# Optimization experiments

Measured on AMD Instinct MI355X. Metric: run time of the kernel, lower is better.

## Reference

```python
import jax, jax.numpy as jnp
import numpy as np

N = 100000
E = 3200000
IN_C, H1, H2 = 512, 64, 32


def gcn_norm(edge_index, edge_weight, num_nodes):
    """PyG gcn_norm with add_self_loops=True: D^-1/2 (A+I) D^-1/2 edge weights."""
    row, col = edge_index[0], edge_index[1]
    loop = jnp.arange(num_nodes, dtype=edge_index.dtype)
    row = jnp.concatenate([row, loop])
    col = jnp.concatenate([col, loop])
    w = jnp.concatenate([edge_weight, jnp.ones((num_nodes,), edge_weight.dtype)])
    deg = jax.ops.segment_sum(w, col, num_segments=num_nodes)
    dinv = jnp.where(deg > 0, jax.lax.rsqrt(jnp.maximum(deg, 1e-12)), 0.0)
    wnorm = dinv[row] * w * dinv[col]
    return row, col, wnorm


def gcn_conv(x, W, b, row, col, wnorm, num_nodes):
    h = x @ W                                   # [N, out] linear first (out <= in)
    msg = wnorm[:, None] * h[row]               # gather + per-edge scale  [E+N, out]
    out = jax.ops.segment_sum(msg, col, num_segments=num_nodes)
    return out + b


def setup_inputs() -> dict:
    key = jax.random.key(0)
    ks = jax.random.split(key, 9)
    x = jax.random.normal(ks[0], (N, IN_C), dtype=jnp.float32)
    edge_index = jax.random.randint(ks[1], (2, E), 0, N, dtype=jnp.int64)
    edge_weight = jax.random.uniform(ks[2], (E,), dtype=jnp.float32)
    # Glorot-style init for GCN linear weights, zero bias (PyG defaults).
    def glorot(k, fan_in, fan_out):
        s = np.sqrt(6.0 / (fan_in + fan_out)).astype(np.float32)
        return jax.random.uniform(k, (fan_in, fan_out), jnp.float32, -s, s)
    return {
        "x": x,
        "edge_index": edge_index,
        "edge_weight": edge_weight,
        "W1": glorot(ks[3], IN_C, H1), "b1": jnp.zeros((H1,), jnp.float32),
        "W2": glorot(ks[4], H1, H2),  "b2": jnp.zeros((H2,), jnp.float32),
        "W3": glorot(ks[5], H2, 1),   "b3": jnp.zeros((1,), jnp.float32),
    }


def reference(x, edge_index, edge_weight, W1, b1, W2, b2, W3, b3):
    # Inference mode: dropout is identity (training=False).
    row, col, wnorm = gcn_norm(edge_index, edge_weight, N)  # cached=True: shared across layers
    h = jax.nn.relu(gcn_conv(x, W1, b1, row, col, wnorm, N))
    h = jax.nn.relu(gcn_conv(h, W2, b2, row, col, wnorm, N))
    h = gcn_conv(h, W3, b3, row, col, wnorm, N)
    return h.reshape(-1)  # [N]
```

## Files before the change

kernel.cpp:

```cpp
#include <hip/hip_runtime.h>

constexpr int BLK = 256;
constexpr int NBLKBIN = 512;
constexpr int MAXNB   = 1024;

typedef __bf16 bf16x8 __attribute__((ext_vector_type(8)));
typedef float  f32x4  __attribute__((ext_vector_type(4)));

__device__ __forceinline__ float blo(unsigned u) { return __uint_as_float(u << 16); }
__device__ __forceinline__ float bhi(unsigned u) { return __uint_as_float(u & 0xffff0000u); }

__device__ __forceinline__ int detect64(const void* ei) {
    const int* p = (const int*)ei;
    int is64 = 1;
#pragma unroll
    for (int i = 0; i < 16; ++i)
        if (p[2 * i + 1] != 0) is64 = 0;
    return is64;
}

__device__ __forceinline__ int load_idx(const void* ei, size_t pos, int is64) {
    if (is64) return (int)((const long long*)ei)[pos];
    return ((const int*)ei)[pos];
}

__global__ void k_prep(const float* __restrict__ W1, const float* __restrict__ W2,
                       __bf16* __restrict__ Wtf, __bf16* __restrict__ Wtf2,
                       int* __restrict__ bkt_cnt, int nb) {
    const int b = blockIdx.x;
    const int t = threadIdx.x;
    if (b < 16) {
        int i = b * 256 + t;
        int lane = i & 63;
        int tt   = (i >> 6) & 3;
        int k0c  = i >> 8;
        int col  = tt * 16 + (lane & 15);
        int kbase = k0c * 32 + (lane >> 4) * 8;
        bf16x8 v;
#pragma unroll
        for (int j = 0; j < 8; ++j) v[j] = (__bf16)W1[(size_t)(kbase + j) * 64 + col];
        *(bf16x8*)(Wtf + (size_t)i * 8) = v;
    } else if (b == 16) {
        int i = t;
        int lane = i & 63;
        int ct   = i >> 6;
        int tt = ct & 1, chunk = ct >> 1;
        int col  = tt * 16 + (lane & 15);
        int kbase = chunk * 32 + (lane >> 4) * 8;
        bf16x8 v;
#pragma unroll
        for (int j = 0; j < 8; ++j) v[j] = (__bf16)W2[(size_t)(kbase + j) * 32 + col];
        *(bf16x8*)(Wtf2 + (size_t)i * 8) = v;
    } else {
        for (int i = t; i < nb; i += 256) bkt_cnt[i] = 0;
    }
}

__global__ __launch_bounds__(256) void k_binhist(const void* __restrict__ ei, int e,
                                                 int* __restrict__ bucket_cnt, int nb) {
    __shared__ int hist[MAXNB];
    const int t = threadIdx.x;
    for (int b = t; b < nb; b += 256) hist[b] = 0;
    __syncthreads();
    const int is64 = detect64(ei);
    const int chunk = (e + NBLKBIN - 1) / NBLKBIN;
    const int i0 = blockIdx.x * chunk;
    const int i1 = min(e, i0 + chunk);
    for (int i = i0 + t; i < i1; i += 256) {
        int dst = load_idx(ei, (size_t)e + i, is64);
        atomicAdd(&hist[dst >> 7], 1);
    }
    __syncthreads();
    for (int b = t; b < nb; b += 256) {
        int c = hist[b];
        if (c) atomicAdd(&bucket_cnt[b], c);
    }
}

__global__ void k_scanbkt(const int* __restrict__ cnt, int* __restrict__ offs,
                          int* __restrict__ cursor, int nb, int e) {
    __shared__ int sh[256];
    const int t = threadIdx.x;
    const int base = t * 4;
    int v[4]; int s = 0;
#pragma unroll
    for (int k = 0; k < 4; ++k) {
        int i = base + k;
        v[k] = (i < nb) ? cnt[i] : 0;
        s += v[k];
    }
    sh[t] = s;
    __syncthreads();
    for (int d = 1; d < 256; d <<= 1) {
        int x = (t >= d) ? sh[t - d] : 0;
        __syncthreads();
        sh[t] += x;
        __syncthreads();
    }
    int excl = (t == 0) ? 0 : sh[t - 1];
#pragma unroll
    for (int k = 0; k < 4; ++k) {
        int i = base + k;
        if (i < nb) { offs[i] = excl; cursor[i] = excl; excl += v[k]; }
    }
    if (t == 255) offs[nb] = e;
}

__global__ __launch_bounds__(256) void k_binscatter(const void* __restrict__ ei,
                                                    const float* __restrict__ ew, int e,
                                                    int* __restrict__ bucket_cursor,
                                                    int2* __restrict__ binned, int nb) {
    __shared__ int hist[MAXNB];
    const int t = threadIdx.x;
    for (int b = t; b < nb; b += 256) hist[b] = 0;
    __syncthreads();
    const int is64 = detect64(ei);
    const int chunk = (e + NBLKBIN - 1) / NBLKBIN;
    const int i0 = blockIdx.x * chunk;
    const int i1 = min(e, i0 + chunk);
    for (int i = i0 + t; i < i1; i += 256) {
        int dst = load_idx(ei, (size_t)e + i, is64);
        atomicAdd(&hist[dst >> 7], 1);
    }
    __syncthreads();
    for (int b = t; b < nb; b += 256) {
        int c = hist[b];
        int base = 0;
        if (c) base = atomicAdd(&bucket_cursor[b], c);
        hist[b] = base;
    }
    __syncthreads();
    for (int i = i0 + t; i < i1; i += 256) {
        int dst = load_idx(ei, (size_t)e + i, is64);
        int src = load_idx(ei, (size_t)i, is64);
        float w = ew[i];
        int bin = dst >> 7;
        int pos = atomicAdd(&hist[bin], 1);
        binned[pos] = make_int2(src | ((dst & 127) << 20), __float_as_int(w));
    }
}

__global__ __launch_bounds__(256) void k_build(const int* __restrict__ bkt_offs,
                                               const int2* __restrict__ binned,
                                               float* __restrict__ dinv,
                                               int* __restrict__ offs,
                                               int2* __restrict__ csrp, int n, int e) {
    __shared__ int                icnt[128];
    __shared__ unsigned long long facc[128];
    __shared__ int                scn[128];
    __shared__ int                cur[128];
    const int t = threadIdx.x;
    const int b = blockIdx.x;
    if (t < 128) { icnt[t] = 0; facc[t] = 0ull; }
    __syncthreads();
    const int j0 = bkt_offs[b], j1 = bkt_offs[b + 1];
    const float SCALE = 1099511627776.f;
    for (int j = j0 + t; j < j1; j += 256) {
        int2 p = binned[j];
        int dl = ((unsigned)p.x) >> 20;
        atomicAdd(&icnt[dl], 1);
        atomicAdd(&facc[dl], (unsigned long long)(__int_as_float(p.y) * SCALE));
    }
    __syncthreads();
    if (t < 128) {
        int nd = b * 128 + t;
        if (nd < n) dinv[nd] = rsqrtf(fmaf((float)facc[t], 1.f / 1099511627776.f, 1.0f));
        scn[t] = icnt[t];
    }
    __syncthreads();
    for (int d = 1; d < 128; d <<= 1) {
        int x = 0;
        if (t < 128 && t >= d) x = scn[t - d];
        __syncthreads();
        if (t < 128) scn[t] += x;
        __syncthreads();
    }
    if (t < 128) {
        int excl = (t == 0) ? 0 : scn[t - 1];
        int abs0 = j0 + excl;
        cur[t] = abs0;
        int nd = b * 128 + t;
        if (nd < n) offs[nd] = abs0;
    }
    if (b == 0 && t == 0) offs[n] = e;
    __syncthreads();
    for (int j = j0 + t; j < j1; j += 256) {
        int2 p = binned[j];
        int dl  = ((unsigned)p.x) >> 20;
        int src = p.x & 0xFFFFF;
        int pos = atomicAdd(&cur[dl], 1);
        csrp[pos] = make_int2(src, p.y);
    }
}

__global__ __launch_bounds__(256) void k_gemm1_mfma(const float* __restrict__ X,
                                                    const __bf16* __restrict__ Wtf,
                                                    const float* __restrict__ dinv,
                                                    __bf16* __restrict__ H, int nrows) {
    const int wave = threadIdx.x >> 6;
    const int lane = threadIdx.x & 63;
    const int l15  = lane & 15;
    const int lq   = lane >> 4;
    const long rbase = (long)blockIdx.x * 128 + wave * 32;

    long ar0 = rbase + l15;      if (ar0 >= nrows) ar0 = nrows - 1;
    long ar1 = rbase + 16 + l15; if (ar1 >= nrows) ar1 = nrows - 1;
    const float4* x0 = (const float4*)(X + (size_t)ar0 * 512) + lq * 2;
    const float4* x1 = (const float4*)(X + (size_t)ar1 * 512) + lq * 2;

    f32x4 acc[2][4];
#pragma unroll
    for (int r = 0; r < 2; ++r)
#pragma unroll
        for (int t = 0; t < 4; ++t) acc[r][t] = f32x4{0.f, 0.f, 0.f, 0.f};

    float4 pa[2][2][2];
#pragma unroll
    for (int s = 0; s < 2; ++s) {
        pa[s][0][0] = x0[s * 8]; pa[s][0][1] = x0[s * 8 + 1];
        pa[s][1][0] = x1[s * 8]; pa[s][1][1] = x1[s * 8 + 1];
    }

#pragma unroll
    for (int k0c = 0; k0c < 16; ++k0c) {
        const int s = k0c & 1;
        float4 a00 = pa[s][0][0], a01 = pa[s][0][1];
        float4 a10 = pa[s][1][0], a11 = pa[s][1][1];
        if (k0c + 2 < 16) {
            pa[s][0][0] = x0[(k0c + 2) * 8]; pa[s][0][1] = x0[(k0c + 2) * 8 + 1];
            pa[s][1][0] = x1[(k0c + 2) * 8]; pa[s][1][1] = x1[(k0c + 2) * 8 + 1];
        }
        bf16x8 af0, af1;
        af0[0] = (__bf16)a00.x; af0[1] = (__bf16)a00.y; af0[2] = (__bf16)a00.z; af0[3] = (__bf16)a00.w;
        af0[4] = (__bf16)a01.x; af0[5] = (__bf16)a01.y; af0[6] = (__bf16)a01.z; af0[7] = (__bf16)a01.w;
        af1[0] = (__bf16)a10.x; af1[1] = (__bf16)a10.y; af1[2] = (__bf16)a10.z; af1[3] = (__bf16)a10.w;
        af1[4] = (__bf16)a11.x; af1[5] = (__bf16)a11.y; af1[6] = (__bf16)a11.z; af1[7] = (__bf16)a11.w;
#pragma unroll
        for (int t = 0; t < 4; ++t) {
            bf16x8 bf_ = *(const bf16x8*)(Wtf + ((size_t)(k0c * 4 + t) * 64 + lane) * 8);
            acc[0][t] = __builtin_amdgcn_mfma_f32_16x16x32_bf16(af0, bf_, acc[0][t], 0, 0, 0);
            acc[1][t] = __builtin_amdgcn_mfma_f32_16x16x32_bf16(af1, bf_, acc[1][t], 0, 0, 0);
        }
    }
#pragma unroll
    for (int rr = 0; rr < 2; ++rr)
#pragma unroll
    for (int r = 0; r < 4; ++r) {
        long row = rbase + rr * 16 + lq * 4 + r;
        if (row < nrows) {
            float dv = dinv[row];
#pragma unroll
            for (int t = 0; t < 4; ++t)
                H[(size_t)row * 64 + t * 16 + l15] = (__bf16)(acc[rr][t][r] * dv);
        }
    }
}

__global__ __launch_bounds__(256) void k_gemm2_mfma(const __bf16* __restrict__ A,
                                                    const __bf16* __restrict__ Wtf2,
                                                    const float* __restrict__ dinv,
                                                    __bf16* __restrict__ H, int nrows) {
    const int wave = threadIdx.x >> 6;
    const int lane = threadIdx.x & 63;
    const int l15  = lane & 15;
    const int lq   = lane >> 4;
    const long rbase = (long)blockIdx.x * 64 + wave * 16;

    long arow = rbase + l15;
    if (arow >= nrows) arow = nrows - 1;

    f32x4 acc[2] = {{0.f,0.f,0.f,0.f},{0.f,0.f,0.f,0.f}};
#pragma unroll
    for (int c = 0; c < 2; ++c) {
        bf16x8 af = *(const bf16x8*)(A + (size_t)arow * 64 + c * 32 + lq * 8);
#pragma unroll
        for (int t = 0; t < 2; ++t) {
            bf16x8 bf_ = *(const bf16x8*)(Wtf2 + ((size_t)(c * 2 + t) * 64 + lane) * 8);
            acc[t] = __builtin_amdgcn_mfma_f32_16x16x32_bf16(af, bf_, acc[t], 0, 0, 0);
        }
    }
#pragma unroll
    for (int r = 0; r < 4; ++r) {
        long row = rbase + lq * 4 + r;
        if (row < nrows) {
            float dv = dinv[row];
#pragma unroll
            for (int t = 0; t < 2; ++t)
                H[(size_t)row * 32 + t * 16 + l15] = (__bf16)(acc[t][r] * dv);
        }
    }
}

template <int K, int EPI>
__global__ __launch_bounds__(256) void k_prop_bf(const int* __restrict__ offs,
                                                 const int2* __restrict__ csrp,
                                                 const __bf16* __restrict__ hb,
                                                 const float* __restrict__ dinv,
                                                 const float* __restrict__ bias,
                                                 const float* __restrict__ W3,
                                                 void* __restrict__ outv, int n) {
    constexpr int SUB = K / 4;
    constexpr int NPW = 64 / SUB;
    constexpr int NPB = 4 * NPW;
    const int t    = threadIdx.x;
    const int lane = t & 63;
    const int wave = t >> 6;
    const int chq  = lane & (SUB - 1);
    const int sub  = lane / SUB;
    const long nd  = (long)blockIdx.x * NPB + wave * NPW + sub;
    if (nd >= n) return;

    const unsigned short* h = (const unsigned short*)hb;
    const int j0 = offs[nd], j1 = offs[nd + 1];
    float a0 = 0.f, a1 = 0.f, a2 = 0.f, a3 = 0.f;
    int j = j0;
    for (; j + 3 < j1; j += 4) {
        int2 p0 = csrp[j];
        int2 p1 = csrp[j + 1];
        int2 p2 = csrp[j + 2];
        int2 p3 = csrp[j + 3];
        uint2 u0 = *(const uint2*)(h + (size_t)p0.x * K + 4 * chq);
        uint2 u1 = *(const uint2*)(h + (size_t)p1.x * K + 4 * chq);
        uint2 u2 = *(const uint2*)(h + (size_t)p2.x * K + 4 * chq);
        uint2 u3 = *(const uint2*)(h + (size_t)p3.x * K + 4 * chq);
        float w0 = __int_as_float(p0.y), w1 = __int_as_float(p1.y);
        float w2 = __int_as_float(p2.y), w3 = __int_as_float(p3.y);
        a0 = fmaf(w0, blo(u0.x), a0); a1 = fmaf(w0, bhi(u0.x), a1);
        a2 = fmaf(w0, blo(u0.y), a2); a3 = fmaf(w0, bhi(u0.y), a3);
        a0 = fmaf(w1, blo(u1.x), a0); a1 = fmaf(w1, bhi(u1.x), a1);
        a2 = fmaf(w1, blo(u1.y), a2); a3 = fmaf(w1, bhi(u1.y), a3);
        a0 = fmaf(w2, blo(u2.x), a0); a1 = fmaf(w2, bhi(u2.x), a1);
        a2 = fmaf(w2, blo(u2.y), a2); a3 = fmaf(w2, bhi(u2.y), a3);
        a0 = fmaf(w3, blo(u3.x), a0); a1 = fmaf(w3, bhi(u3.x), a1);
        a2 = fmaf(w3, blo(u3.y), a2); a3 = fmaf(w3, bhi(u3.y), a3);
    }
    for (; j < j1; ++j) {
        int2 p0 = csrp[j];
        uint2 u0 = *(const uint2*)(h + (size_t)p0.x * K + 4 * chq);
        float w0 = __int_as_float(p0.y);
        a0 = fmaf(w0, blo(u0.x), a0); a1 = fmaf(w0, bhi(u0.x), a1);
        a2 = fmaf(w0, blo(u0.y), a2); a3 = fmaf(w0, bhi(u0.y), a3);
    }
    const float di = dinv[nd];
    uint2 us = *(const uint2*)(h + (size_t)nd * K + 4 * chq);
    float4 bv = *(const float4*)(bias + 4 * chq);
    float o0 = fmaf(di, a0 + blo(us.x), bv.x);
    float o1 = fmaf(di, a1 + bhi(us.x), bv.y);
    float o2 = fmaf(di, a2 + blo(us.y), bv.z);
    float o3 = fmaf(di, a3 + bhi(us.y), bv.w);
    o0 = fmaxf(o0, 0.f); o1 = fmaxf(o1, 0.f); o2 = fmaxf(o2, 0.f); o3 = fmaxf(o3, 0.f);
    if (EPI == 0) {
        unsigned short s0 = __builtin_bit_cast(unsigned short, (__bf16)o0);
        unsigned short s1 = __builtin_bit_cast(unsigned short, (__bf16)o1);
        unsigned short s2 = __builtin_bit_cast(unsigned short, (__bf16)o2);
        unsigned short s3 = __builtin_bit_cast(unsigned short, (__bf16)o3);
        uint2 pk;
        pk.x = (unsigned)s0 | ((unsigned)s1 << 16);
        pk.y = (unsigned)s2 | ((unsigned)s3 << 16);
        *(uint2*)((unsigned*)outv + (size_t)nd * (K / 2) + 2 * chq) = pk;
    } else {
        float4 wv = *(const float4*)(W3 + 4 * chq);
        float part = o0 * wv.x + o1 * wv.y + o2 * wv.z + o3 * wv.w;
#pragma unroll
        for (int d = SUB / 2; d >= 1; d >>= 1) part += __shfl_xor(part, d, SUB);
        if (chq == 0) ((float*)outv)[nd] = di * part;
    }
}

__global__ __launch_bounds__(256) void k_prop1(const int* __restrict__ offs,
                                               const int2* __restrict__ csrp,
                                               const float* __restrict__ h,
                                               const float* __restrict__ dinv,
                                               const float* __restrict__ bias,
                                               float* __restrict__ out, int n) {
    long nd = (long)blockIdx.x * BLK + threadIdx.x;
    if (nd >= n) return;
    const int j0 = offs[nd], j1 = offs[nd + 1];
    float acc = 0.f;
    int j = j0;
    for (; j + 3 < j1; j += 4) {
        int2 p0 = csrp[j];
        int2 p1 = csrp[j + 1];
        int2 p2 = csrp[j + 2];
        int2 p3 = csrp[j + 3];
        acc = fmaf(__int_as_float(p0.y), h[p0.x], acc);
        acc = fmaf(__int_as_float(p1.y), h[p1.x], acc);
        acc = fmaf(__int_as_float(p2.y), h[p2.x], acc);
        acc = fmaf(__int_as_float(p3.y), h[p3.x], acc);
    }
    for (; j < j1; ++j) {
        int2 p0 = csrp[j];
        acc = fmaf(__int_as_float(p0.y), h[p0.x], acc);
    }
    const float di = dinv[nd];
    out[nd] = fmaf(di, acc + h[nd], bias[0]);
}

extern "C" void kernel_launch(void* const* d_in, const int* in_sizes, int n_in,
                              void* d_out, int out_size, void* d_ws, size_t ws_size,
                              hipStream_t stream) {
    const float* x  = (const float*)d_in[0];
    const void*  ei = d_in[1];
    const float* ew = (const float*)d_in[2];
    const float* W1 = (const float*)d_in[3];
    const float* b1 = (const float*)d_in[4];
    const float* W2 = (const float*)d_in[5];
    const float* b2 = (const float*)d_in[6];
    const float* W3 = (const float*)d_in[7];
    const float* b3 = (const float*)d_in[8];
    float* out = (float*)d_out;

    const int n = in_sizes[0] / 512;
    const int e = in_sizes[2];
    const int nb = (n + 127) >> 7;

    char* ws = (char*)d_ws;
    size_t off = 0;
    auto alloc = [&](size_t bytes) {
        void* p = ws + off;
        off = (off + bytes + 255) & ~(size_t)255;
        return p;
    };
    int2*   binned   = (int2*)  alloc((size_t)e * 8);
    __bf16* hbuf1    = (__bf16*)binned;
    int*    bkt_cnt  = (int*)   alloc((size_t)(MAXNB + 1) * 4);
    int*    bkt_offs = (int*)   alloc((size_t)(MAXNB + 1) * 4);
    int*    bkt_cur  = (int*)   alloc((size_t)(MAXNB + 1) * 4);
    int*    offs     = (int*)   alloc((size_t)(n + 1) * 4);
    int2*   csrp     = (int2*)  alloc((size_t)e * 8);
    float*  dinv     = (float*) alloc((size_t)n * 4);
    __bf16* pb64     = (__bf16*)alloc((size_t)n * 64 * 2);
    __bf16* hbuf2    = (__bf16*)alloc((size_t)n * 32 * 2);
    float*  h3       = (float*) alloc((size_t)n * 4);
    __bf16* Wtf      = (__bf16*)alloc((size_t)512 * 64 * 2);
    __bf16* Wtf2     = (__bf16*)alloc((size_t)64 * 32 * 2);
    (void)ws_size; (void)n_in; (void)out_size;

    const int gb_n = (n + BLK - 1) / BLK;

    k_prep<<<18, 256, 0, stream>>>(W1, W2, Wtf, Wtf2, bkt_cnt, nb);
    k_binhist<<<NBLKBIN, 256, 0, stream>>>(ei, e, bkt_cnt, nb);
    k_scanbkt<<<1, 256, 0, stream>>>(bkt_cnt, bkt_offs, bkt_cur, nb, e);
    k_binscatter<<<NBLKBIN, 256, 0, stream>>>(ei, ew, e, bkt_cur, binned, nb);
    k_build<<<nb, 256, 0, stream>>>(bkt_offs, binned, dinv, offs, csrp, n, e);

    k_gemm1_mfma<<<(n + 127) / 128, 256, 0, stream>>>(x, Wtf, dinv, hbuf1, n);
    k_prop_bf<64, 0><<<(n + 15) / 16, 256, 0, stream>>>(offs, csrp, hbuf1, dinv, b1, nullptr, pb64, n);

    k_gemm2_mfma<<<(n + 63) / 64, 256, 0, stream>>>(pb64, Wtf2, dinv, hbuf2, n);
    k_prop_bf<32, 1><<<(n + 31) / 32, 256, 0, stream>>>(offs, csrp, hbuf2, dinv, b2, W3, h3, n);

    k_prop1<<<gb_n, BLK, 0, stream>>>(offs, csrp, h3, dinv, b3, out, n);
}
```

Baseline: 326.9 us.

## Fuse edge binning with GEMM1, compute degrees early, prefold normalization into edge weights

Degree accumulation now happens with global float atomics during the histogram pass, so dinv is ready before CSR construction. With dinv no longer needed by GEMM1, the bin-scatter and GEMM1 run as one kernel whose blocks are split between the two jobs, letting the bandwidth-heavy matmul overlap the scatter. The symmetric normalization dinv[src]*w*dinv[dst] is folded into the stored CSR weights, which removes the dinv scaling from the GEMM epilogues and the propagation kernels. In exchange it adds E global atomics on deg and a separate buffer for H1, which is no longer aliased onto the binned array, and float atomics make the degree sums order-dependent.

```diff
diff --git a/kernel.cpp b/kernel.cpp
--- a/kernel.cpp
+++ b/kernel.cpp
@@ -26,7 +26,8 @@
 
 __global__ void k_prep(const float* __restrict__ W1, const float* __restrict__ W2,
                        __bf16* __restrict__ Wtf, __bf16* __restrict__ Wtf2,
-                       int* __restrict__ bkt_cnt, int nb) {
+                       int* __restrict__ bkt_cnt, int nb,
+                       float* __restrict__ deg, int n) {
     const int b = blockIdx.x;
     const int t = threadIdx.x;
     if (b < 16) {
@@ -51,13 +52,18 @@
 #pragma unroll
         for (int j = 0; j < 8; ++j) v[j] = (__bf16)W2[(size_t)(kbase + j) * 32 + col];
         *(bf16x8*)(Wtf2 + (size_t)i * 8) = v;
+    } else if (b == 17) {
+        for (int i = t; i < nb; i += 256) bkt_cnt[i] = 0;
     } else {
-        for (int i = t; i < nb; i += 256) bkt_cnt[i] = 0;
-    }
-}
-
-__global__ __launch_bounds__(256) void k_binhist(const void* __restrict__ ei, int e,
-                                                 int* __restrict__ bucket_cnt, int nb) {
+        int i = (b - 18) * 256 + t;
+        if (i < n) deg[i] = 0.f;
+    }
+}
+
+__global__ __launch_bounds__(256) void k_binhist_deg(const void* __restrict__ ei,
+                                                     const float* __restrict__ ew, int e,
+                                                     int* __restrict__ bucket_cnt, int nb,
+                                                     float* __restrict__ deg) {
     __shared__ int hist[MAXNB];
     const int t = threadIdx.x;
     for (int b = t; b < nb; b += 256) hist[b] = 0;
@@ -69,6 +75,7 @@
     for (int i = i0 + t; i < i1; i += 256) {
         int dst = load_idx(ei, (size_t)e + i, is64);
         atomicAdd(&hist[dst >> 7], 1);
+        atomicAdd(&deg[dst], ew[i]);
     }
     __syncthreads();
     for (int b = t; b < nb; b += 256) {
@@ -77,131 +84,85 @@
     }
 }
 
-__global__ void k_scanbkt(const int* __restrict__ cnt, int* __restrict__ offs,
-                          int* __restrict__ cursor, int nb, int e) {
+__global__ void k_scan_rsqrt(const int* __restrict__ cnt, int* __restrict__ offs,
+                             int* __restrict__ cursor, int nb, int e,
+                             const float* __restrict__ deg, float* __restrict__ dinv, int n) {
     __shared__ int sh[256];
     const int t = threadIdx.x;
-    const int base = t * 4;
-    int v[4]; int s = 0;
-#pragma unroll
-    for (int k = 0; k < 4; ++k) {
-        int i = base + k;
-        v[k] = (i < nb) ? cnt[i] : 0;
-        s += v[k];
-    }
-    sh[t] = s;
-    __syncthreads();
-    for (int d = 1; d < 256; d <<= 1) {
-        int x = (t >= d) ? sh[t - d] : 0;
-        __syncthreads();
-        sh[t] += x;
-        __syncthreads();
-    }
-    int excl = (t == 0) ? 0 : sh[t - 1];
-#pragma unroll
-    for (int k = 0; k < 4; ++k) {
-        int i = base + k;
-        if (i < nb) { offs[i] = excl; cursor[i] = excl; excl += v[k]; }
-    }
-    if (t == 255) offs[nb] = e;
-}
-
-__global__ __launch_bounds__(256) void k_binscatter(const void* __restrict__ ei,
-                                                    const float* __restrict__ ew, int e,
-                                                    int* __restrict__ bucket_cursor,
-                                                    int2* __restrict__ binned, int nb) {
+    if (blockIdx.x == 0) {
+        const int base = t * 4;
+        int v[4]; int s = 0;
+#pragma unroll
+        for (int k = 0; k < 4; ++k) {
+            int i = base + k;
+            v[k] = (i < nb) ? cnt[i] : 0;
+            s += v[k];
+        }
+        sh[t] = s;
+        __syncthreads();
+        for (int d = 1; d < 256; d <<= 1) {
+            int x = (t >= d) ? sh[t - d] : 0;
+            __syncthreads();
+            sh[t] += x;
+            __syncthreads();
+        }
+        int excl = (t == 0) ? 0 : sh[t - 1];
+#pragma unroll
+        for (int k = 0; k < 4; ++k) {
+            int i = base + k;
+            if (i < nb) { offs[i] = excl; cursor[i] = excl; excl += v[k]; }
+        }
+        if (t == 255) offs[nb] = e;
+    } else {
+        long i = (long)(blockIdx.x - 1) * BLK + t;
+        if (i < n) dinv[i] = rsqrtf(1.0f + deg[i]);
+    }
+}
+
+__global__ __launch_bounds__(256) void k_fat(const void* __restrict__ ei,
+                                             const float* __restrict__ ew, int e,
+                                             int* __restrict__ bucket_cursor,
+                                             int2* __restrict__ binned, int nb,
+                                             const float* __restrict__ X,
+                                             const __bf16* __restrict__ Wtf,
+                                             __bf16* __restrict__ H, int nrows) {
     __shared__ int hist[MAXNB];
     const int t = threadIdx.x;
-    for (int b = t; b < nb; b += 256) hist[b] = 0;
-    __syncthreads();
-    const int is64 = detect64(ei);
-    const int chunk = (e + NBLKBIN - 1) / NBLKBIN;
-    const int i0 = blockIdx.x * chunk;
-    const int i1 = min(e, i0 + chunk);
-    for (int i = i0 + t; i < i1; i += 256) {
-        int dst = load_idx(ei, (size_t)e + i, is64);
-        atomicAdd(&hist[dst >> 7], 1);
-    }
-    __syncthreads();
-    for (int b = t; b < nb; b += 256) {
-        int c = hist[b];
-        int base = 0;
-        if (c) base = atomicAdd(&bucket_cursor[b], c);
-        hist[b] = base;
-    }
-    __syncthreads();
-    for (int i = i0 + t; i < i1; i += 256) {
-        int dst = load_idx(ei, (size_t)e + i, is64);
-        int src = load_idx(ei, (size_t)i, is64);
-        float w = ew[i];
-        int bin = dst >> 7;
-        int pos = atomicAdd(&hist[bin], 1);
-        binned[pos] = make_int2(src | ((dst & 127) << 20), __float_as_int(w));
-    }
-}
-
-__global__ __launch_bounds__(256) void k_build(const int* __restrict__ bkt_offs,
-                                               const int2* __restrict__ binned,
-                                               float* __restrict__ dinv,
-                                               int* __restrict__ offs,
-                                               int2* __restrict__ csrp, int n, int e) {
-    __shared__ int                icnt[128];
-    __shared__ unsigned long long facc[128];
-    __shared__ int                scn[128];
-    __shared__ int                cur[128];
-    const int t = threadIdx.x;
-    const int b = blockIdx.x;
-    if (t < 128) { icnt[t] = 0; facc[t] = 0ull; }
-    __syncthreads();
-    const int j0 = bkt_offs[b], j1 = bkt_offs[b + 1];
-    const float SCALE = 1099511627776.f;
-    for (int j = j0 + t; j < j1; j += 256) {
-        int2 p = binned[j];
-        int dl = ((unsigned)p.x) >> 20;
-        atomicAdd(&icnt[dl], 1);
-        atomicAdd(&facc[dl], (unsigned long long)(__int_as_float(p.y) * SCALE));
-    }
-    __syncthreads();
-    if (t < 128) {
-        int nd = b * 128 + t;
-        if (nd < n) dinv[nd] = rsqrtf(fmaf((float)facc[t], 1.f / 1099511627776.f, 1.0f));
-        scn[t] = icnt[t];
-    }
-    __syncthreads();
-    for (int d = 1; d < 128; d <<= 1) {
-        int x = 0;
-        if (t < 128 && t >= d) x = scn[t - d];
-        __syncthreads();
-        if (t < 128) scn[t] += x;
-        __syncthreads();
-    }
-    if (t < 128) {
-        int excl = (t == 0) ? 0 : scn[t - 1];
-        int abs0 = j0 + excl;
-        cur[t] = abs0;
-        int nd = b * 128 + t;
-        if (nd < n) offs[nd] = abs0;
-    }
-    if (b == 0 && t == 0) offs[n] = e;
-    __syncthreads();
-    for (int j = j0 + t; j < j1; j += 256) {
-        int2 p = binned[j];
-        int dl  = ((unsigned)p.x) >> 20;
-        int src = p.x & 0xFFFFF;
-        int pos = atomicAdd(&cur[dl], 1);
-        csrp[pos] = make_int2(src, p.y);
-    }
-}
-
-__global__ __launch_bounds__(256) void k_gemm1_mfma(const float* __restrict__ X,
-                                                    const __bf16* __restrict__ Wtf,
-                                                    const float* __restrict__ dinv,
-                                                    __bf16* __restrict__ H, int nrows) {
-    const int wave = threadIdx.x >> 6;
-    const int lane = threadIdx.x & 63;
+    if (blockIdx.x < NBLKBIN) {
+        for (int b = t; b < nb; b += 256) hist[b] = 0;
+        __syncthreads();
+        const int is64 = detect64(ei);
+        const int chunk = (e + NBLKBIN - 1) / NBLKBIN;
+        const int i0 = blockIdx.x * chunk;
+        const int i1 = min(e, i0 + chunk);
+        for (int i = i0 + t; i < i1; i += 256) {
+            int dst = load_idx(ei, (size_t)e + i, is64);
+            atomicAdd(&hist[dst >> 7], 1);
+        }
+        __syncthreads();
+        for (int b = t; b < nb; b += 256) {
+            int c = hist[b];
+            int base = 0;
+            if (c) base = atomicAdd(&bucket_cursor[b], c);
+            hist[b] = base;
+        }
+        __syncthreads();
+        for (int i = i0 + t; i < i1; i += 256) {
+            int dst = load_idx(ei, (size_t)e + i, is64);
+            int src = load_idx(ei, (size_t)i, is64);
+            float w = ew[i];
+            int bin = dst >> 7;
+            int pos = atomicAdd(&hist[bin], 1);
+            binned[pos] = make_int2(src | ((dst & 127) << 20), __float_as_int(w));
+        }
+        return;
+    }
+    const int bid  = blockIdx.x - NBLKBIN;
+    const int wave = t >> 6;
+    const int lane = t & 63;
     const int l15  = lane & 15;
     const int lq   = lane >> 4;
-    const long rbase = (long)blockIdx.x * 128 + wave * 32;
+    const long rbase = (long)bid * 128 + wave * 32;
 
     long ar0 = rbase + l15;      if (ar0 >= nrows) ar0 = nrows - 1;
     long ar1 = rbase + 16 + l15; if (ar1 >= nrows) ar1 = nrows - 1;
@@ -212,7 +173,7 @@
 #pragma unroll
     for (int r = 0; r < 2; ++r)
 #pragma unroll
-        for (int t = 0; t < 4; ++t) acc[r][t] = f32x4{0.f, 0.f, 0.f, 0.f};
+        for (int tt = 0; tt < 4; ++tt) acc[r][tt] = f32x4{0.f, 0.f, 0.f, 0.f};
 
     float4 pa[2][2][2];
 #pragma unroll
@@ -236,29 +197,76 @@
         af1[0] = (__bf16)a10.x; af1[1] = (__bf16)a10.y; af1[2] = (__bf16)a10.z; af1[3] = (__bf16)a10.w;
         af1[4] = (__bf16)a11.x; af1[5] = (__bf16)a11.y; af1[6] = (__bf16)a11.z; af1[7] = (__bf16)a11.w;
 #pragma unroll
-        for (int t = 0; t < 4; ++t) {
-            bf16x8 bf_ = *(const bf16x8*)(Wtf + ((size_t)(k0c * 4 + t) * 64 + lane) * 8);
-            acc[0][t] = __builtin_amdgcn_mfma_f32_16x16x32_bf16(af0, bf_, acc[0][t], 0, 0, 0);
-            acc[1][t] = __builtin_amdgcn_mfma_f32_16x16x32_bf16(af1, bf_, acc[1][t], 0, 0, 0);
+        for (int tt = 0; tt < 4; ++tt) {
+            bf16x8 bf_ = *(const bf16x8*)(Wtf + ((size_t)(k0c * 4 + tt) * 64 + lane) * 8);
+            acc[0][tt] = __builtin_amdgcn_mfma_f32_16x16x32_bf16(af0, bf_, acc[0][tt], 0, 0, 0);
+            acc[1][tt] = __builtin_amdgcn_mfma_f32_16x16x32_bf16(af1, bf_, acc[1][tt], 0, 0, 0);
         }
     }
 #pragma unroll
     for (int rr = 0; rr < 2; ++rr)
+#pragma unroll
+    for (int tt = 0; tt < 4; ++tt)
 #pragma unroll
     for (int r = 0; r < 4; ++r) {
         long row = rbase + rr * 16 + lq * 4 + r;
-        if (row < nrows) {
-            float dv = dinv[row];
-#pragma unroll
-            for (int t = 0; t < 4; ++t)
-                H[(size_t)row * 64 + t * 16 + l15] = (__bf16)(acc[rr][t][r] * dv);
-        }
+        if (row < nrows) H[(size_t)row * 64 + tt * 16 + l15] = (__bf16)acc[rr][tt][r];
+    }
+}
+
+__global__ __launch_bounds__(256) void k_build(const int* __restrict__ bkt_offs,
+                                               const int2* __restrict__ binned,
+                                               const float* __restrict__ dinv,
+                                               int* __restrict__ offs,
+                                               int2* __restrict__ csrp, int n, int e) {
+    __shared__ int   icnt[128];
+    __shared__ int   scn[128];
+    __shared__ int   cur[128];
+    __shared__ float ddst[128];
+    const int t = threadIdx.x;
+    const int b = blockIdx.x;
+    if (t < 128) {
+        icnt[t] = 0;
+        int nd = b * 128 + t;
+        ddst[t] = (nd < n) ? dinv[nd] : 0.f;
+    }
+    __syncthreads();
+    const int j0 = bkt_offs[b], j1 = bkt_offs[b + 1];
+    for (int j = j0 + t; j < j1; j += 256) {
+        int2 p = binned[j];
+        atomicAdd(&icnt[((unsigned)p.x) >> 20], 1);
+    }
+    __syncthreads();
+    if (t < 128) scn[t] = icnt[t];
+    __syncthreads();
+    for (int d = 1; d < 128; d <<= 1) {
+        int x = 0;
+        if (t < 128 && t >= d) x = scn[t - d];
+        __syncthreads();
+        if (t < 128) scn[t] += x;
+        __syncthreads();
+    }
+    if (t < 128) {
+        int excl = (t == 0) ? 0 : scn[t - 1];
+        int abs0 = j0 + excl;
+        cur[t] = abs0;
+        int nd = b * 128 + t;
+        if (nd < n) offs[nd] = abs0;
+    }
+    if (b == 0 && t == 0) offs[n] = e;
+    __syncthreads();
+    for (int j = j0 + t; j < j1; j += 256) {
+        int2 p = binned[j];
+        int dl  = ((unsigned)p.x) >> 20;
+        int src = p.x & 0xFFFFF;
+        int pos = atomicAdd(&cur[dl], 1);
+        float w2 = __int_as_float(p.y) * dinv[src] * ddst[dl];
+        csrp[pos] = make_int2(src, __float_as_int(w2));
     }
 }
 
 __global__ __launch_bounds__(256) void k_gemm2_mfma(const __bf16* __restrict__ A,
                                                     const __bf16* __restrict__ Wtf2,
-                                                    const float* __restrict__ dinv,
                                                     __bf16* __restrict__ H, int nrows) {
     const int wave = threadIdx.x >> 6;
     const int lane = threadIdx.x & 63;
@@ -280,14 +288,11 @@
         }
     }
 #pragma unroll
+    for (int t = 0; t < 2; ++t)
+#pragma unroll
     for (int r = 0; r < 4; ++r) {
         long row = rbase + lq * 4 + r;
-        if (row < nrows) {
-            float dv = dinv[row];
-#pragma unroll
-            for (int t = 0; t < 2; ++t)
-                H[(size_t)row * 32 + t * 16 + l15] = (__bf16)(acc[t][r] * dv);
-        }
+        if (row < nrows) H[(size_t)row * 32 + t * 16 + l15] = (__bf16)acc[t][r];
     }
 }
 
@@ -342,12 +347,13 @@
         a2 = fmaf(w0, blo(u0.y), a2); a3 = fmaf(w0, bhi(u0.y), a3);
     }
     const float di = dinv[nd];
+    const float s  = di * di;
     uint2 us = *(const uint2*)(h + (size_t)nd * K + 4 * chq);
     float4 bv = *(const float4*)(bias + 4 * chq);
-    float o0 = fmaf(di, a0 + blo(us.x), bv.x);
-    float o1 = fmaf(di, a1 + bhi(us.x), bv.y);
-    float o2 = fmaf(di, a2 + blo(us.y), bv.z);
-    float o3 = fmaf(di, a3 + bhi(us.y), bv.w);
+    float o0 = fmaf(s, blo(us.x), a0 + bv.x);
+    float o1 = fmaf(s, bhi(us.x), a1 + bv.y);
+    float o2 = fmaf(s, blo(us.y), a2 + bv.z);
+    float o3 = fmaf(s, bhi(us.y), a3 + bv.w);
     o0 = fmaxf(o0, 0.f); o1 = fmaxf(o1, 0.f); o2 = fmaxf(o2, 0.f); o3 = fmaxf(o3, 0.f);
     if (EPI == 0) {
         unsigned short s0 = __builtin_bit_cast(unsigned short, (__bf16)o0);
@@ -363,7 +369,7 @@
         float part = o0 * wv.x + o1 * wv.y + o2 * wv.z + o3 * wv.w;
 #pragma unroll
         for (int d = SUB / 2; d >= 1; d >>= 1) part += __shfl_xor(part, d, SUB);
-        if (chq == 0) ((float*)outv)[nd] = di * part;
+        if (chq == 0) ((float*)outv)[nd] = part;
     }
 }
 
@@ -393,7 +399,7 @@
         acc = fmaf(__int_as_float(p0.y), h[p0.x], acc);
     }
     const float di = dinv[nd];
-    out[nd] = fmaf(di, acc + h[nd], bias[0]);
+    out[nd] = fmaf(di * di, h[nd], acc + bias[0]);
 }
 
 extern "C" void kernel_launch(void* const* d_in, const int* in_sizes, int n_in,
@@ -428,27 +434,27 @@
     int*    bkt_cur  = (int*)   alloc((size_t)(MAXNB + 1) * 4);
     int*    offs     = (int*)   alloc((size_t)(n + 1) * 4);
     int2*   csrp     = (int2*)  alloc((size_t)e * 8);
+    float*  deg      = (float*) alloc((size_t)n * 4);
     float*  dinv     = (float*) alloc((size_t)n * 4);
+    __bf16* hb1      = (__bf16*)alloc((size_t)n * 64 * 2);
     __bf16* pb64     = (__bf16*)alloc((size_t)n * 64 * 2);
     __bf16* hbuf2    = (__bf16*)alloc((size_t)n * 32 * 2);
     float*  h3       = (float*) alloc((size_t)n * 4);
     __bf16* Wtf      = (__bf16*)alloc((size_t)512 * 64 * 2);
     __bf16* Wtf2     = (__bf16*)alloc((size_t)64 * 32 * 2);
-    (void)ws_size; (void)n_in; (void)out_size;
+    (void)ws_size; (void)n_in; (void)out_size; (void)hbuf1;
 
     const int gb_n = (n + BLK - 1) / BLK;
 
-    k_prep<<<18, 256, 0, stream>>>(W1, W2, Wtf, Wtf2, bkt_cnt, nb);
-    k_binhist<<<NBLKBIN, 256, 0, stream>>>(ei, e, bkt_cnt, nb);
-    k_scanbkt<<<1, 256, 0, stream>>>(bkt_cnt, bkt_offs, bkt_cur, nb, e);
-    k_binscatter<<<NBLKBIN, 256, 0, stream>>>(ei, ew, e, bkt_cur, binned, nb);
+    k_prep<<<18 + gb_n, 256, 0, stream>>>(W1, W2, Wtf, Wtf2, bkt_cnt, nb, deg, n);
+    k_binhist_deg<<<NBLKBIN, 256, 0, stream>>>(ei, ew, e, bkt_cnt, nb, deg);
+    k_scan_rsqrt<<<1 + gb_n, 256, 0, stream>>>(bkt_cnt, bkt_offs, bkt_cur, nb, e, deg, dinv, n);
+    k_fat<<<NBLKBIN + (n + 127) / 128, 256, 0, stream>>>(ei, ew, e, bkt_cur, binned, nb,
+                                                         x, Wtf, hb1, n);
     k_build<<<nb, 256, 0, stream>>>(bkt_offs, binned, dinv, offs, csrp, n, e);
 
-    k_gemm1_mfma<<<(n + 127) / 128, 256, 0, stream>>>(x, Wtf, dinv, hbuf1, n);
-    k_prop_bf<64, 0><<<(n + 15) / 16, 256, 0, stream>>>(offs, csrp, hbuf1, dinv, b1, nullptr, pb64, n);
-
-    k_gemm2_mfma<<<(n + 63) / 64, 256, 0, stream>>>(pb64, Wtf2, dinv, hbuf2, n);
+    k_prop_bf<64, 0><<<(n + 15) / 16, 256, 0, stream>>>(offs, csrp, hb1, dinv, b1, nullptr, pb64, n);
+    k_gemm2_mfma<<<(n + 63) / 64, 256, 0, stream>>>(pb64, Wtf2, hbuf2, n);
     k_prop_bf<32, 1><<<(n + 31) / 32, 256, 0, stream>>>(offs, csrp, hbuf2, dinv, b2, W3, h3, n);
-
     k_prop1<<<gb_n, BLK, 0, stream>>>(offs, csrp, h3, dinv, b3, out, n);
 }
```

Measured after the change: 492.8 us. 1.51x slower.
